# Kernel tuning notes

Hardware: AMD Instinct MI355X
Metric: run time of the kernel (lower is better)

Reference implementation:

```python
import jax, jax.numpy as jnp
import numpy as np


def setup_inputs() -> dict:
    key = jax.random.key(0)
    k1, k2, k3 = jax.random.split(key, 3)
    B, D, F = 4096, 1024, 16384  # batch, input_dim, dict_size
    x = jax.random.normal(k1, (B, D), dtype=jnp.float32)
    W_enc = jax.random.normal(k2, (F, D), dtype=jnp.float32) * (1.0 / np.sqrt(D))
    b_enc = jnp.zeros((F,), dtype=jnp.float32)
    W_dec = jax.random.normal(k3, (D, F), dtype=jnp.float32)
    # decoder columns are unit-normalized (as in _normalize_decoder)
    W_dec = W_dec / jnp.clip(jnp.linalg.norm(W_dec, axis=0, keepdims=True), 1e-8)
    b_dec = jnp.zeros((D,), dtype=jnp.float32)
    return {"x": x, "W_enc": W_enc, "b_enc": b_enc, "W_dec": W_dec, "b_dec": b_dec, "k": 32}


def reference(x, W_enc, b_enc, W_dec, b_dec, k):
    # encode: z_pre = (x - b_dec) @ W_enc^T + b_enc   -> [B, F]
    x_centered = x - b_dec
    z_pre = jnp.einsum('bd,fd->bf', x_centered, W_enc) + b_enc
    # activate: TopK(ReLU(z_pre)) via top_k + relu + scatter
    topk_vals, topk_idx = jax.lax.top_k(z_pre, k)           # [B, k]
    B = z_pre.shape[0]
    rows = jnp.arange(B)[:, None]                            # [B, 1]
    z = jnp.zeros_like(z_pre).at[rows, topk_idx].set(jax.nn.relu(topk_vals))
    # decode: x_hat = z @ W_dec^T + b_dec (dense matmul over sparse z)
    x_hat = jnp.einsum('bf,df->bd', z, W_dec) + b_dec
    return (x_hat, z, z_pre)
```

## Files before the change

### kernel.cpp

```cpp
#include <hip/hip_runtime.h>
#include <cstdint>
#include <cfloat>
#include <cstddef>

#define MAXK 128

typedef __attribute__((ext_vector_type(8))) short bf16x8;
typedef __attribute__((ext_vector_type(4))) float f32x4;

__device__ __forceinline__ void split8(const float4& v0, const float4& v1,
                                       uint4& hp, uint4& lp)
{
    float vv[8] = {v0.x, v0.y, v0.z, v0.w, v1.x, v1.y, v1.z, v1.w};
    unsigned h[8], l[8];
    #pragma unroll
    for (int i = 0; i < 8; ++i) {
        unsigned u  = __float_as_uint(vv[i]);
        unsigned hb = u & 0xFFFF0000u;
        float lf    = vv[i] - __uint_as_float(hb);
        h[i] = u;
        l[i] = __float_as_uint(lf);
    }
    hp.x = (h[0] >> 16) | (h[1] & 0xFFFF0000u);
    hp.y = (h[2] >> 16) | (h[3] & 0xFFFF0000u);
    hp.z = (h[4] >> 16) | (h[5] & 0xFFFF0000u);
    hp.w = (h[6] >> 16) | (h[7] & 0xFFFF0000u);
    lp.x = (l[0] >> 16) | (l[1] & 0xFFFF0000u);
    lp.y = (l[2] >> 16) | (l[3] & 0xFFFF0000u);
    lp.z = (l[4] >> 16) | (l[5] & 0xFFFF0000u);
    lp.w = (l[6] >> 16) | (l[7] & 0xFFFF0000u);
}

__device__ __forceinline__ void gload_lds16(const void* g, void* l)
{
    __builtin_amdgcn_global_load_lds(
        (const __attribute__((address_space(1))) unsigned int*)g,
        (__attribute__((address_space(3))) unsigned int*)l,
        16, 0, 0);
}

__global__ __launch_bounds__(256)
void prep_x_kernel(const float* __restrict__ x, const float* __restrict__ b_dec,
                   ushort* __restrict__ AhiP, ushort* __restrict__ AloP, int D)
{
    const int c   = blockIdx.x * 256 + threadIdx.x;
    const int t   = c >> 9;
    const int wc  = c & 511;
    const int rl  = wc >> 2;
    const int pkc = wc & 3;
    const int kc  = (pkc - (rl >> 1)) & 3;
    const int nkb = D >> 5;
    const int band = t / nkb, kblk = t - band * nkb;
    const int row = band * 128 + rl;
    const int k0  = kblk * 32 + kc * 8;

    const float* src = x + (size_t)row * D + k0;
    float4 v0 = *(const float4*)(src);
    float4 v1 = *(const float4*)(src + 4);
    const float* bd = b_dec + k0;
    float4 d0 = *(const float4*)(bd);
    float4 d1 = *(const float4*)(bd + 4);
    v0.x -= d0.x; v0.y -= d0.y; v0.z -= d0.z; v0.w -= d0.w;
    v1.x -= d1.x; v1.y -= d1.y; v1.z -= d1.z; v1.w -= d1.w;
    uint4 hp, lp;
    split8(v0, v1, hp, lp);
    const size_t off = (size_t)t * 4096 + (size_t)wc * 8;
    *(uint4*)&AhiP[off] = hp;
    *(uint4*)&AloP[off] = lp;
}

__global__ __launch_bounds__(256)
void prep_w_kernel(const float* __restrict__ Wenc,
                   ushort* __restrict__ WhiP, ushort* __restrict__ WloP, int D)
{
    const int c   = blockIdx.x * 256 + threadIdx.x;
    const int t   = c >> 10;
    const int wc  = c & 1023;
    const int rl  = wc >> 2;
    const int pkc = wc & 3;
    const int kc  = (pkc - (rl >> 1)) & 3;
    const int nkb = D >> 5;
    const int fband = t / nkb, kblk = t - fband * nkb;
    const int f   = fband * 256 + rl;
    const int k0  = kblk * 32 + kc * 8;

    const float* src = Wenc + (size_t)f * D + k0;
    float4 v0 = *(const float4*)(src);
    float4 v1 = *(const float4*)(src + 4);
    uint4 hp, lp;
    split8(v0, v1, hp, lp);
    const size_t off = (size_t)t * 8192 + (size_t)wc * 8;
    *(uint4*)&WhiP[off] = hp;
    *(uint4*)&WloP[off] = lp;
}

__global__ __launch_bounds__(256, 2)
void encode_gemm_pre(const ushort* __restrict__ AhiP, const ushort* __restrict__ AloP,
                     const ushort* __restrict__ WhiP, const ushort* __restrict__ WloP,
                     const float* __restrict__ b_enc, float* __restrict__ z_pre,
                     int D, int F)
{
    __shared__ ushort AsHi[4096];
    __shared__ ushort AsLo[4096];
    __shared__ ushort BsHi[8192];
    __shared__ ushort BsLo[8192];

    const int tid = threadIdx.x;
    const int bm  = blockIdx.y * 128;
    const int bn  = blockIdx.x * 256;

    const int lane = tid & 63;
    const int w    = tid >> 6;
    const int wm   = (w >> 1) * 64;
    const int wn   = (w & 1) * 128;
    const int fr   = lane & 15;
    const int q    = lane >> 4;
    const int nkb  = D >> 5;

    int aoff[4], boff[8];
    #pragma unroll
    for (int mi = 0; mi < 4; ++mi) {
        const int r = wm + mi * 16 + fr;
        aoff[mi] = r * 32 + (((q + (r >> 1)) & 3) * 8);
    }
    #pragma unroll
    for (int ni = 0; ni < 8; ++ni) {
        const int r = wn + ni * 16 + fr;
        boff[ni] = r * 32 + (((q + (r >> 1)) & 3) * 8);
    }

    f32x4 acc[4][8];
    #pragma unroll
    for (int mi = 0; mi < 4; ++mi)
        #pragma unroll
        for (int ni = 0; ni < 8; ++ni)
            acc[mi][ni] = (f32x4){0.f, 0.f, 0.f, 0.f};

    const char* aHi = (const char*)AhiP + (size_t)blockIdx.y * nkb * 8192;
    const char* aLo = (const char*)AloP + (size_t)blockIdx.y * nkb * 8192;
    const char* bHi = (const char*)WhiP + (size_t)blockIdx.x * nkb * 16384;
    const char* bLo = (const char*)WloP + (size_t)blockIdx.x * nkb * 16384;
    const int la16 = lane * 16;

    for (int kb = 0; kb < nkb; ++kb) {
        const char* pa = aHi + (size_t)kb * 8192;
        const char* pl = aLo + (size_t)kb * 8192;
        const char* pb = bHi + (size_t)kb * 16384;
        const char* pm = bLo + (size_t)kb * 16384;

        #pragma unroll
        for (int c = 0; c < 2; ++c) {
            const int off = (w * 2 + c) * 1024;
            gload_lds16(pa + off + la16, (char*)AsHi + off);
            gload_lds16(pl + off + la16, (char*)AsLo + off);
        }
        #pragma unroll
        for (int c = 0; c < 4; ++c) {
            const int off = (w * 4 + c) * 1024;
            gload_lds16(pb + off + la16, (char*)BsHi + off);
            gload_lds16(pm + off + la16, (char*)BsLo + off);
        }
        asm volatile("s_waitcnt vmcnt(0)" ::: "memory");
        __syncthreads();

        bf16x8 ahi[4], alo[4];
        #pragma unroll
        for (int mi = 0; mi < 4; ++mi) {
            ahi[mi] = *(const bf16x8*)&AsHi[aoff[mi]];
            alo[mi] = *(const bf16x8*)&AsLo[aoff[mi]];
        }
        #pragma unroll
        for (int ni = 0; ni < 8; ++ni) {
            bf16x8 bhi = *(const bf16x8*)&BsHi[boff[ni]];
            bf16x8 blo = *(const bf16x8*)&BsLo[boff[ni]];
            #pragma unroll
            for (int mi = 0; mi < 4; ++mi) {
                acc[mi][ni] = __builtin_amdgcn_mfma_f32_16x16x32_bf16(alo[mi], bhi, acc[mi][ni], 0, 0, 0);
                acc[mi][ni] = __builtin_amdgcn_mfma_f32_16x16x32_bf16(ahi[mi], blo, acc[mi][ni], 0, 0, 0);
                acc[mi][ni] = __builtin_amdgcn_mfma_f32_16x16x32_bf16(ahi[mi], bhi, acc[mi][ni], 0, 0, 0);
            }
        }
        __syncthreads();
    }

    #pragma unroll
    for (int ni = 0; ni < 8; ++ni) {
        const int col = bn + wn + ni * 16 + fr;
        const float be = b_enc[col];
        #pragma unroll
        for (int mi = 0; mi < 4; ++mi) {
            const int rbase = bm + wm + mi * 16 + q * 4;
            float* dst = z_pre + (size_t)rbase * F + col;
            #pragma unroll
            for (int r = 0; r < 4; ++r)
                dst[(size_t)r * F] = acc[mi][ni][r] + be;
        }
    }
}

__global__ __launch_bounds__(256, 2)
void encode_gemm_bf16x3(const float* __restrict__ x, const float* __restrict__ Wenc,
                        const float* __restrict__ b_enc, const float* __restrict__ b_dec,
                        float* __restrict__ z_pre, int D, int F)
{
    constexpr int BM = 128, BN = 256, BK = 32;
    __shared__ ushort AsHi[BM * BK];
    __shared__ ushort AsLo[BM * BK];
    __shared__ ushort BsHi[BN * BK];
    __shared__ ushort BsLo[BN * BK];

    const int tid = threadIdx.x;
    const int bm  = blockIdx.y * BM;
    const int bn  = blockIdx.x * BN;

    const int lane = tid & 63;
    const int w    = tid >> 6;
    const int wm   = (w >> 1) * 64;
    const int wn   = (w & 1) * 128;
    const int fr   = lane & 15;
    const int q    = lane >> 4;

    int aoff[4], boff[8];
    #pragma unroll
    for (int mi = 0; mi < 4; ++mi) {
        const int r = wm + mi * 16 + fr;
        aoff[mi] = r * 32 + (((q + (r >> 1)) & 3) * 8);
    }
    #pragma unroll
    for (int ni = 0; ni < 8; ++ni) {
        const int r = wn + ni * 16 + fr;
        boff[ni] = r * 32 + (((q + (r >> 1)) & 3) * 8);
    }

    f32x4 acc[4][8];
    #pragma unroll
    for (int mi = 0; mi < 4; ++mi)
        #pragma unroll
        for (int ni = 0; ni < 8; ++ni)
            acc[mi][ni] = (f32x4){0.f, 0.f, 0.f, 0.f};

    for (int k0 = 0; k0 < D; k0 += BK) {
        #pragma unroll
        for (int j = 0; j < 2; ++j) {
            const int task = tid + 256 * j;
            const int row = task >> 2, kc = task & 3;
            const float* src = x + (size_t)(bm + row) * D + k0 + kc * 8;
            float4 v0 = *(const float4*)(src);
            float4 v1 = *(const float4*)(src + 4);
            const float* bd = b_dec + k0 + kc * 8;
            float4 d0 = *(const float4*)(bd);
            float4 d1 = *(const float4*)(bd + 4);
            v0.x -= d0.x; v0.y -= d0.y; v0.z -= d0.z; v0.w -= d0.w;
            v1.x -= d1.x; v1.y -= d1.y; v1.z -= d1.z; v1.w -= d1.w;
            uint4 hp, lp;
            split8(v0, v1, hp, lp);
            const int off = row * 32 + (((kc + (row >> 1)) & 3) * 8);
            *(uint4*)&AsHi[off] = hp;
            *(uint4*)&AsLo[off] = lp;
        }
        #pragma unroll
        for (int j = 0; j < 4; ++j) {
            const int task = tid + 256 * j;
            const int row = task >> 2, kc = task & 3;
            const float* src = Wenc + (size_t)(bn + row) * D + k0 + kc * 8;
            float4 v0 = *(const float4*)(src);
            float4 v1 = *(const float4*)(src + 4);
            uint4 hp, lp;
            split8(v0, v1, hp, lp);
            const int off = row * 32 + (((kc + (row >> 1)) & 3) * 8);
            *(uint4*)&BsHi[off] = hp;
            *(uint4*)&BsLo[off] = lp;
        }
        __syncthreads();

        bf16x8 ahi[4], alo[4];
        #pragma unroll
        for (int mi = 0; mi < 4; ++mi) {
            ahi[mi] = *(const bf16x8*)&AsHi[aoff[mi]];
            alo[mi] = *(const bf16x8*)&AsLo[aoff[mi]];
        }
        #pragma unroll
        for (int ni = 0; ni < 8; ++ni) {
            bf16x8 bhi = *(const bf16x8*)&BsHi[boff[ni]];
            bf16x8 blo = *(const bf16x8*)&BsLo[boff[ni]];
            #pragma unroll
            for (int mi = 0; mi < 4; ++mi) {
                acc[mi][ni] = __builtin_amdgcn_mfma_f32_16x16x32_bf16(alo[mi], bhi, acc[mi][ni], 0, 0, 0);
                acc[mi][ni] = __builtin_amdgcn_mfma_f32_16x16x32_bf16(ahi[mi], blo, acc[mi][ni], 0, 0, 0);
                acc[mi][ni] = __builtin_amdgcn_mfma_f32_16x16x32_bf16(ahi[mi], bhi, acc[mi][ni], 0, 0, 0);
            }
        }
        __syncthreads();
    }

    #pragma unroll
    for (int ni = 0; ni < 8; ++ni) {
        const int col = bn + wn + ni * 16 + fr;
        const float be = b_enc[col];
        #pragma unroll
        for (int mi = 0; mi < 4; ++mi) {
            const int rbase = bm + wm + mi * 16 + q * 4;
            float* dst = z_pre + (size_t)rbase * F + col;
            #pragma unroll
            for (int r = 0; r < 4; ++r)
                dst[(size_t)r * F] = acc[mi][ni][r] + be;
        }
    }
}

__device__ __forceinline__ unsigned fkey(float f)
{
    unsigned u = __float_as_uint(f);
    return u ^ ((unsigned)((int)u >> 31) | 0x80000000u);
}
__device__ __forceinline__ float finv(unsigned k)
{
    unsigned u = (k & 0x80000000u) ? (k ^ 0x80000000u) : ~k;
    return __uint_as_float(u);
}

__device__ __forceinline__ float exact_zpre(const float* __restrict__ xr,
                                            const float* __restrict__ Wenc,
                                            const float* __restrict__ b_enc,
                                            const float* __restrict__ b_dec,
                                            int f, int D, int ln)
{
    const float* wr = Wenc + (size_t)f * D;
    float s = 0.f;
    for (int d = ln * 4; d < D; d += 256) {
        float4 xv = *(const float4*)(xr + d);
        float4 bd = *(const float4*)(b_dec + d);
        float4 wv4 = *(const float4*)(wr + d);
        s = fmaf(xv.x - bd.x, wv4.x, s);
        s = fmaf(xv.y - bd.y, wv4.y, s);
        s = fmaf(xv.z - bd.z, wv4.z, s);
        s = fmaf(xv.w - bd.w, wv4.w, s);
    }
    #pragma unroll
    for (int o = 32; o > 0; o >>= 1) s += __shfl_down(s, o, 64);
    return s + b_enc[f];
}

#define DLT 4e-3f

template <int NVEC>
__global__ __launch_bounds__(256)
void topk_fast(const float* __restrict__ z_pre, float* __restrict__ z,
               float* __restrict__ ws_vals, int* __restrict__ ws_idx,
               const int* __restrict__ k_ptr,
               const float* __restrict__ x, const float* __restrict__ Wenc,
               const float* __restrict__ b_enc, const float* __restrict__ b_dec,
               int F, int D)
{
    const int row = blockIdx.x;
    const int t   = threadIdx.x;
    const int k   = *k_ptr;
    const int nv4 = F >> 2;
    const int wv_id = t >> 6, ln = t & 63;

    __shared__ ushort keys[16384];
    __shared__ float  cand_v[256];
    __shared__ int    cand_i[256];
    __shared__ unsigned char cand_sel[256];
    __shared__ int    bnd[128];
    __shared__ float  s2w[4];
    __shared__ int    hist4[4][256];
    __shared__ int    waveTot[4];
    __shared__ int    s_bin, s_above;
    __shared__ int    n_c_s, n_b_s, c_hi_s, out_cnt, cnt_tau_s, bad_s;
    __shared__ unsigned vk_key;

    if (t == 0) {
        n_c_s = 0; n_b_s = 0; c_hi_s = 0; out_cnt = 0; cnt_tau_s = 0; bad_s = 0;
        vk_key = 0xFFFFFFFFu;
    }

    const float*  zrow = z_pre + (size_t)row * F;
    const float4* src  = (const float4*)zrow;

    float s2 = 0.f;
    #pragma unroll
    for (int i = 0; i < NVEC; ++i) {
        const int p = t + 256 * i;
        if (p < nv4) {
            const float4 v = src[p];
            const unsigned k0 = fkey(v.x) >> 16;
            const unsigned k1 = fkey(v.y) >> 16;
            const unsigned k2 = fkey(v.z) >> 16;
            const unsigned k3 = fkey(v.w) >> 16;
            uint2 pk;
            pk.x = k0 | (k1 << 16);
            pk.y = k2 | (k3 << 16);
            *(uint2*)&keys[p * 4] = pk;
            s2 = fmaf(v.x, v.x, s2);
            s2 = fmaf(v.y, v.y, s2);
            s2 = fmaf(v.z, v.z, s2);
            s2 = fmaf(v.w, v.w, s2);
        }
    }
    #pragma unroll
    for (int o = 32; o > 0; o >>= 1) s2 += __shfl_down(s2, o, 64);
    if (ln == 0) s2w[wv_id] = s2;
    __syncthreads();

    const float sigma = sqrtf((s2w[0] + s2w[1] + s2w[2] + s2w[3]) / (float)F);
    int c0 = 4 * k; if (c0 < 64) c0 = 64; if (c0 > 192) c0 = 192;
    const float qq  = (float)c0 / (float)F;
    const float tt  = sqrtf(-2.f * logf(qq));
    const float phi = tt - (2.30753f + 0.27061f * tt) /
                           (1.f + 0.99229f * tt + 0.04481f * tt * tt);
    const float tau = sigma * phi;
    const unsigned tk = fkey(tau) >> 16;
    const unsigned tkey16 = (tk >= 2) ? (tk - 2) : 0;

    const int nU = nv4 * 2;
    const unsigned* keysU = (const unsigned*)keys;
    for (int j = t; j < nU; j += 256) {
        const unsigned pr = keysU[j];
        const unsigned ka = pr & 0xFFFFu, kb = pr >> 16;
        if (ka > tkey16) { const int s = atomicAdd(&n_c_s, 1); if (s < 256) cand_i[s] = 2 * j; }
        if (kb > tkey16) { const int s = atomicAdd(&n_c_s, 1); if (s < 256) cand_i[s] = 2 * j + 1; }
    }
    __syncthreads();

    if (t == 0 && (n_c_s > 256 || !(tau > 0.1f))) bad_s = 1;
    const int n_c = min(n_c_s, 256);

    float myv = 0.f;
    if (t < n_c) {
        myv = zrow[cand_i[t]];
        cand_v[t] = myv;
        if (myv > tau) atomicAdd(&cnt_tau_s, 1);
    }
    __syncthreads();
    if (t == 0 && cnt_tau_s < k) bad_s = 1;

    cand_sel[t] = 0;
    if (t < n_c) {
        int gt = 0;
        for (int j = 0; j < n_c; ++j) gt += (cand_v[j] > myv);
        if (gt <= k - 1) atomicMin(&vk_key, fkey(myv));
    }
    __syncthreads();

    const float vkv = finv(vk_key);
    if (t < n_c) {
        if (myv > vkv + DLT) {
            cand_sel[t] = 2;
            atomicAdd(&c_hi_s, 1);
        } else if (myv > vkv - DLT) {
            const int sb = atomicAdd(&n_b_s, 1);
            if (sb < 128) bnd[sb] = t;
        }
    }
    __syncthreads();
    if (t == 0 && n_b_s > 128) bad_s = 1;
    __syncthreads();

    if (!bad_s) {
        const int n_b = n_b_s;
        const float* xr = x + (size_t)row * D;
        for (int b2 = wv_id; b2 < n_b; b2 += 4) {
            const int c = bnd[b2];
            const float ex = exact_zpre(xr, Wenc, b_enc, b_dec, cand_i[c], D, ln);
            if (ln == 0) cand_v[c] = ex;
        }
        __syncthreads();

        if (t == 0) {
            int need = k - c_hi_s;
            if (need > n_b) need = n_b;
            for (int it = 0; it < need; ++it) {
                int bi = -1; float bv = 0.f;
                for (int b2 = 0; b2 < n_b; ++b2) {
                    const int c = bnd[b2];
                    if (cand_sel[c]) continue;
                    const float v = cand_v[c];
                    if (bi < 0 || v > bv || (v == bv && cand_i[c] < cand_i[bi])) {
                        bi = c; bv = v;
                    }
                }
                if (bi < 0) break;
                cand_sel[bi] = 1;
            }
        }
        __syncthreads();

        float4* dstz = (float4*)(z + (size_t)row * F);
        const float4 zz = make_float4(0.f, 0.f, 0.f, 0.f);
        #pragma unroll
        for (int i = 0; i < NVEC; ++i) {
            const int p = t + 256 * i;
            if (p < nv4) dstz[p] = zz;
        }
        __syncthreads();

        float* wvp = ws_vals + (size_t)row * MAXK;
        int*   wip = ws_idx  + (size_t)row * MAXK;
        if (t < n_c && cand_sel[t]) {
            const float zv = fmaxf(cand_v[t], 0.f);
            z[(size_t)row * F + cand_i[t]] = zv;
            const int s = atomicAdd(&out_cnt, 1);
            if (s < MAXK) { wvp[s] = zv; wip[s] = cand_i[t]; }
        }
        return;
    }

    if (t == 0) { n_c_s = 0; c_hi_s = 0; out_cnt = 0; }
    __syncthreads();

    unsigned prefix = 0;
    int rem = k;
    for (int pass = 0; pass < 2; ++pass) {
        const int shift = 24 - 8 * pass;
        hist4[0][t] = 0; hist4[1][t] = 0; hist4[2][t] = 0; hist4[3][t] = 0;
        __syncthreads();
        for (int j = t; j < F; j += 256) {
            const unsigned key = fkey(zrow[j]);
            const bool inb = (pass == 0) || ((key >> (shift + 8)) == prefix);
            if (inb) atomicAdd(&hist4[wv_id][(key >> shift) & 255], 1);
        }
        __syncthreads();
        const int cnt = hist4[0][t] + hist4[1][t] + hist4[2][t] + hist4[3][t];
        int s = cnt;
        #pragma unroll
        for (int off = 1; off < 64; off <<= 1) {
            const int tmp = __shfl_down(s, off, 64);
            if (ln + off < 64) s += tmp;
        }
        if (ln == 0) waveTot[wv_id] = s;
        __syncthreads();
        int add = 0;
        #pragma unroll
        for (int w2 = 0; w2 < 4; ++w2)
            if (w2 > wv_id) add += waveTot[w2];
        const int sfx = s + add;
        const int nxt = sfx - cnt;
        if (sfx >= rem && nxt < rem) { s_bin = t; s_above = nxt; }
        __syncthreads();
        rem -= s_above;
        prefix = (prefix << 8) | (unsigned)s_bin;
        __syncthreads();
    }

    const float hiT = finv((prefix << 16) | 0xFFFFu) + DLT;
    const float loT = finv(prefix << 16) - DLT;

    for (int j = t; j < F; j += 256) {
        const float v = zrow[j];
        if (v > hiT) atomicAdd(&c_hi_s, 1);
        else if (v > loT) {
            const int s = atomicAdd(&n_c_s, 1);
            if (s < 256) { cand_i[s] = j; cand_sel[s] = 0; }
        }
    }
    __syncthreads();
    const int n_c2 = min(n_c_s, 256);

    {
        const float* xr = x + (size_t)row * D;
        for (int c = wv_id; c < n_c2; c += 4) {
            const float ex = exact_zpre(xr, Wenc, b_enc, b_dec, cand_i[c], D, ln);
            if (ln == 0) cand_v[c] = ex;
        }
    }
    __syncthreads();

    if (t == 0) {
        int need = k - c_hi_s;
        if (need > n_c2) need = n_c2;
        for (int it = 0; it < need; ++it) {
            int bi = -1; float bv = 0.f;
            for (int c = 0; c < n_c2; ++c) {
                if (cand_sel[c]) continue;
                const float v = cand_v[c];
                if (bi < 0 || v > bv || (v == bv && cand_i[c] < cand_i[bi])) {
                    bi = c; bv = v;
                }
            }
            if (bi < 0) break;
            cand_sel[bi] = 1;
        }
    }
    __syncthreads();

    {
        float4* dstz = (float4*)(z + (size_t)row * F);
        const float4 zz = make_float4(0.f, 0.f, 0.f, 0.f);
        #pragma unroll
        for (int i = 0; i < NVEC; ++i) {
            const int p = t + 256 * i;
            if (p < nv4) dstz[p] = zz;
        }
    }
    __syncthreads();

    float* wvp = ws_vals + (size_t)row * MAXK;
    int*   wip = ws_idx  + (size_t)row * MAXK;
    for (int j = t; j < F; j += 256) {
        const float v = zrow[j];
        if (v > hiT) {
            const float zv = fmaxf(v, 0.f);
            z[(size_t)row * F + j] = zv;
            const int s = atomicAdd(&out_cnt, 1);
            if (s < MAXK) { wvp[s] = zv; wip[s] = j; }
        }
    }
    if (t < n_c2 && cand_sel[t]) {
        const float zv = fmaxf(cand_v[t], 0.f);
        z[(size_t)row * F + cand_i[t]] = zv;
        const int s = atomicAdd(&out_cnt, 1);
        if (s < MAXK) { wvp[s] = zv; wip[s] = cand_i[t]; }
    }
}

template <int NVEC>
__global__ __launch_bounds__(256)
void topk_kernel(const float* __restrict__ z_pre, float* __restrict__ z,
                 float* __restrict__ ws_vals, int* __restrict__ ws_idx,
                 const int* __restrict__ k_ptr,
                 const float* __restrict__ x, const float* __restrict__ Wenc,
                 const float* __restrict__ b_enc, const float* __restrict__ b_dec,
                 int F, int D)
{
    const int row = blockIdx.x;
    const int t   = threadIdx.x;
    const int k   = *k_ptr;
    const int nv4 = F >> 2;
    const int wv_id = t >> 6;
    const int ln    = t & 63;

    const float4* src = (const float4*)(z_pre + (size_t)row * F);
    float4 vals[NVEC];
    #pragma unroll
    for (int i = 0; i < NVEC; ++i) {
        const int p = t + 256 * i;
        if (p < nv4) vals[i] = src[p];
        else         vals[i] = make_float4(-FLT_MAX, -FLT_MAX, -FLT_MAX, -FLT_MAX);
    }

    __shared__ int hist[4][256];
    __shared__ int waveTot[4];
    __shared__ int s_bin, s_above;
    __shared__ int c_hi_s, n_c_s, out_cnt;
    __shared__ int cand_idx[128];
    __shared__ float cand_val[128];
    __shared__ unsigned char cand_sel[128];

    unsigned prefix = 0;
    int rem = k;

    #pragma unroll
    for (int pass = 0; pass < 2; ++pass) {
        const int shift = 24 - 8 * pass;
        hist[0][t] = 0; hist[1][t] = 0; hist[2][t] = 0; hist[3][t] = 0;
        __syncthreads();
        #pragma unroll
        for (int i = 0; i < NVEC; ++i) {
            const float* vv = (const float*)&vals[i];
            #pragma unroll
            for (int j = 0; j < 4; ++j) {
                const unsigned key = fkey(vv[j]);
                const bool inb = (pass == 0) || ((key >> (shift + 8)) == prefix);
                if (inb) atomicAdd(&hist[wv_id][(key >> shift) & 255], 1);
            }
        }
        __syncthreads();
        const int cnt = hist[0][t] + hist[1][t] + hist[2][t] + hist[3][t];
        int s = cnt;
        #pragma unroll
        for (int off = 1; off < 64; off <<= 1) {
            const int tmp = __shfl_down(s, off, 64);
            if (ln + off < 64) s += tmp;
        }
        if (ln == 0) waveTot[wv_id] = s;
        __syncthreads();
        int add = 0;
        #pragma unroll
        for (int w2 = 0; w2 < 4; ++w2)
            if (w2 > wv_id) add += waveTot[w2];
        const int sfx = s + add;
        const int nxt = sfx - cnt;
        if (sfx >= rem && nxt < rem) { s_bin = t; s_above = nxt; }
        __syncthreads();
        rem -= s_above;
        prefix = (prefix << 8) | (unsigned)s_bin;
        __syncthreads();
    }

    const unsigned keyLo = prefix << 16;
    const unsigned keyHi = keyLo | 0xFFFFu;
    const float dlt = 1e-3f;
    const float hiThr = finv(keyHi) + dlt;
    const float loThr = finv(keyLo) - dlt;

    if (t == 0) { c_hi_s = 0; n_c_s = 0; out_cnt = 0; }
    __syncthreads();

    #pragma unroll
    for (int i = 0; i < NVEC; ++i) {
        const float* vv = (const float*)&vals[i];
        #pragma unroll
        for (int j = 0; j < 4; ++j) {
            const float v = vv[j];
            if (v > hiThr) {
                atomicAdd(&c_hi_s, 1);
            } else if (v > loThr) {
                const int s = atomicAdd(&n_c_s, 1);
                if (s < 128) { cand_idx[s] = (t + 256 * i) * 4 + j; cand_sel[s] = 0; }
            }
        }
    }
    __syncthreads();

    const int n_c = min(n_c_s, 128);

    {
        const float* xr = x + (size_t)row * D;
        for (int c = wv_id; c < n_c; c += 4) {
            const float ex = exact_zpre(xr, Wenc, b_enc, b_dec, cand_idx[c], D, ln);
            if (ln == 0) cand_val[c] = ex;
        }
    }
    __syncthreads();

    if (t == 0) {
        int need = k - c_hi_s;
        if (need > n_c) need = n_c;
        for (int it = 0; it < need; ++it) {
            int bi = -1; float bv = 0.f;
            for (int c = 0; c < n_c; ++c) {
                if (cand_sel[c]) continue;
                const float v = cand_val[c];
                if (bi < 0 || v > bv || (v == bv && cand_idx[c] < cand_idx[bi])) {
                    bi = c; bv = v;
                }
            }
            if (bi < 0) break;
            cand_sel[bi] = 1;
        }
    }
    __syncthreads();

    float4* dstz = (float4*)(z + (size_t)row * F);
    float*  wv   = ws_vals + (size_t)row * MAXK;
    int*    wi   = ws_idx  + (size_t)row * MAXK;

    #pragma unroll
    for (int i = 0; i < NVEC; ++i) {
        const int p4 = t + 256 * i;
        if (p4 < nv4) {
            const float* vv = (const float*)&vals[i];
            float4 outv;
            float* ov = (float*)&outv;
            #pragma unroll
            for (int j = 0; j < 4; ++j) {
                const int pos = p4 * 4 + j;
                const float v = vv[j];
                float zv = 0.f;
                bool sel = false;
                if (v > hiThr) {
                    zv = fmaxf(v, 0.f); sel = true;
                } else if (v > loThr) {
                    for (int c = 0; c < n_c; ++c) {
                        if (cand_idx[c] == pos) {
                            if (cand_sel[c]) { zv = fmaxf(cand_val[c], 0.f); sel = true; }
                            break;
                        }
                    }
                }
                ov[j] = zv;
                if (sel) {
                    const int s = atomicAdd(&out_cnt, 1);
                    if (s < MAXK) { wv[s] = zv; wi[s] = pos; }
                }
            }
            dstz[p4] = outv;
        }
    }
}

__global__ __launch_bounds__(256)
void transpose_kernel(const float* __restrict__ in, float* __restrict__ out,
                      int R, int C)
{
    __shared__ float tile[32][33];
    const int c0 = blockIdx.x * 32;
    const int r0 = blockIdx.y * 32;
    const int tx = threadIdx.x & 31;
    const int ty = threadIdx.x >> 5;

    #pragma unroll
    for (int i = ty; i < 32; i += 8) {
        const int r = r0 + i, c = c0 + tx;
        tile[i][tx] = (r < R && c < C) ? in[(size_t)r * C + c] : 0.f;
    }
    __syncthreads();
    #pragma unroll
    for (int i = ty; i < 32; i += 8) {
        const int c = c0 + i, r = r0 + tx;
        if (c < C && r < R) out[(size_t)c * R + r] = tile[tx][i];
    }
}

__global__ __launch_bounds__(256)
void decode_kernel(const float* __restrict__ WdT, const float* __restrict__ wvals,
                   const int* __restrict__ widx, const float* __restrict__ b_dec,
                   float* __restrict__ x_hat, const int* __restrict__ k_ptr, int D)
{
    __shared__ float sv[MAXK];
    __shared__ int   si[MAXK];
    const int row = blockIdx.x;
    const int t   = threadIdx.x;
    int k = *k_ptr;
    if (k > MAXK) k = MAXK;

    if (t < MAXK) {
        sv[t] = wvals[(size_t)row * MAXK + t];
        si[t] = widx [(size_t)row * MAXK + t];
    }
    __syncthreads();

    for (int d0 = t * 4; d0 < D; d0 += 1024) {
        float4 acc0 = *(const float4*)(b_dec + d0);
        float4 acc1 = make_float4(0.f, 0.f, 0.f, 0.f);
        int j = 0;
        for (; j + 2 <= k; j += 2) {
            const float v0 = sv[j],     v1 = sv[j + 1];
            const int   f0 = si[j],     f1 = si[j + 1];
            const float4 w0 = *(const float4*)(WdT + (size_t)f0 * D + d0);
            const float4 w1 = *(const float4*)(WdT + (size_t)f1 * D + d0);
            acc0.x = fmaf(v0, w0.x, acc0.x);
            acc0.y = fmaf(v0, w0.y, acc0.y);
            acc0.z = fmaf(v0, w0.z, acc0.z);
            acc0.w = fmaf(v0, w0.w, acc0.w);
            acc1.x = fmaf(v1, w1.x, acc1.x);
            acc1.y = fmaf(v1, w1.y, acc1.y);
            acc1.z = fmaf(v1, w1.z, acc1.z);
            acc1.w = fmaf(v1, w1.w, acc1.w);
        }
        if (j < k) {
            const float v0 = sv[j];
            const float4 w0 = *(const float4*)(WdT + (size_t)si[j] * D + d0);
            acc0.x = fmaf(v0, w0.x, acc0.x);
            acc0.y = fmaf(v0, w0.y, acc0.y);
            acc0.z = fmaf(v0, w0.z, acc0.z);
            acc0.w = fmaf(v0, w0.w, acc0.w);
        }
        acc0.x += acc1.x; acc0.y += acc1.y; acc0.z += acc1.z; acc0.w += acc1.w;
        *(float4*)(x_hat + (size_t)row * D + d0) = acc0;
    }
}

extern "C" void kernel_launch(void* const* d_in, const int* in_sizes, int n_in,
                              void* d_out, int out_size, void* d_ws, size_t ws_size,
                              hipStream_t stream)
{
    const float* x     = (const float*)d_in[0];
    const float* W_enc = (const float*)d_in[1];
    const float* b_enc = (const float*)d_in[2];
    const float* W_dec = (const float*)d_in[3];
    const float* b_dec = (const float*)d_in[4];
    const int*   k_ptr = (const int*)d_in[5];

    const int F = in_sizes[2];
    const int D = in_sizes[4];
    const int B = in_sizes[0] / D;

    float* x_hat = (float*)d_out;
    float* z     = x_hat + (size_t)B * D;
    float* z_pre = z + (size_t)B * F;

    float* WdT = (float*)d_ws;
    float* wv  = WdT + (size_t)F * D;
    int*   wi  = (int*)(wv + (size_t)B * MAXK);
    char*  extra = (char*)(wi + (size_t)B * MAXK);

    const size_t base_need  = (size_t)F * D * 4 + (size_t)B * MAXK * 8;
    const size_t extra_need = (size_t)B * D * 4 + (size_t)F * D * 4;
    const bool use_pre = (ws_size >= base_need + extra_need) &&
                         (D % 32 == 0) && (B % 128 == 0) && (F % 256 == 0);

    if (use_pre) {
        ushort* AhiP = (ushort*)extra;
        ushort* AloP = AhiP + (size_t)B * D;
        ushort* WhiP = AloP + (size_t)B * D;
        ushort* WloP = WhiP + (size_t)F * D;

        prep_x_kernel<<<(B * (D / 8)) / 256, 256, 0, stream>>>(x, b_dec, AhiP, AloP, D);
        prep_w_kernel<<<(F * (D / 8)) / 256, 256, 0, stream>>>(W_enc, WhiP, WloP, D);
        encode_gemm_pre<<<dim3(F / 256, B / 128), 256, 0, stream>>>(
            AhiP, AloP, WhiP, WloP, b_enc, z_pre, D, F);
    } else {
        encode_gemm_bf16x3<<<dim3(F / 256, B / 128), 256, 0, stream>>>(
            x, W_enc, b_enc, b_dec, z_pre, D, F);
    }

    transpose_kernel<<<dim3((F + 31) / 32, (D + 31) / 32), 256, 0, stream>>>(
        W_dec, WdT, D, F);

    const int nv4  = F / 4;
    const int nvec = (nv4 + 255) / 256;
    const bool fastok = (F <= 16384) && ((F & 3) == 0);

    if (fastok) {
        if (nvec <= 4)
            topk_fast<4><<<B, 256, 0, stream>>>(z_pre, z, wv, wi, k_ptr, x, W_enc, b_enc, b_dec, F, D);
        else if (nvec <= 8)
            topk_fast<8><<<B, 256, 0, stream>>>(z_pre, z, wv, wi, k_ptr, x, W_enc, b_enc, b_dec, F, D);
        else
            topk_fast<16><<<B, 256, 0, stream>>>(z_pre, z, wv, wi, k_ptr, x, W_enc, b_enc, b_dec, F, D);
    } else {
        if (nvec <= 8)
            topk_kernel<8><<<B, 256, 0, stream>>>(z_pre, z, wv, wi, k_ptr, x, W_enc, b_enc, b_dec, F, D);
        else if (nvec <= 16)
            topk_kernel<16><<<B, 256, 0, stream>>>(z_pre, z, wv, wi, k_ptr, x, W_enc, b_enc, b_dec, F, D);
        else
            topk_kernel<32><<<B, 256, 0, stream>>>(z_pre, z, wv, wi, k_ptr, x, W_enc, b_enc, b_dec, F, D);
    }

    decode_kernel<<<B, 256, 0, stream>>>(WdT, wv, wi, b_dec, x_hat, k_ptr, D);
}
```

Measured before the change: 1.119 ms.

## Add double-buffered encode GEMM with XCD-aware block swizzle; fuse z zeroing into load

```diff
diff --git a/kernel.cpp b/kernel.cpp
--- a/kernel.cpp
+++ b/kernel.cpp
@@ -92,6 +92,130 @@
     const size_t off = (size_t)t * 8192 + (size_t)wc * 8;
     *(uint4*)&WhiP[off] = hp;
     *(uint4*)&WloP[off] = lp;
+}
+
+__global__ __launch_bounds__(256, 1)
+void encode_gemm_db(const ushort* __restrict__ AhiP, const ushort* __restrict__ AloP,
+                    const ushort* __restrict__ WhiP, const ushort* __restrict__ WloP,
+                    const float* __restrict__ b_enc, float* __restrict__ z_pre,
+                    int D, int F, int nbm)
+{
+    __shared__ ushort AsHi0[4096], AsLo0[4096];
+    __shared__ ushort BsHi0[8192], BsLo0[8192];
+    __shared__ ushort AsHi1[4096], AsLo1[4096];
+    __shared__ ushort BsHi1[8192], BsLo1[8192];
+
+    const int tid = threadIdx.x;
+    const int nwg = gridDim.x;
+    int lb = blockIdx.x;
+    if ((nwg & 7) == 0) {
+        const int per = nwg >> 3;
+        lb = (blockIdx.x & 7) * per + (blockIdx.x >> 3);
+    }
+    const int bm = (lb % nbm) * 128;
+    const int bn = (lb / nbm) * 256;
+
+    const int lane = tid & 63;
+    const int w    = tid >> 6;
+    const int wm   = (w >> 1) * 64;
+    const int wn   = (w & 1) * 128;
+    const int fr   = lane & 15;
+    const int q    = lane >> 4;
+    const int nkb  = D >> 5;
+
+    int aoff[4], boff[8];
+    #pragma unroll
+    for (int mi = 0; mi < 4; ++mi) {
+        const int r = wm + mi * 16 + fr;
+        aoff[mi] = r * 32 + (((q + (r >> 1)) & 3) * 8);
+    }
+    #pragma unroll
+    for (int ni = 0; ni < 8; ++ni) {
+        const int r = wn + ni * 16 + fr;
+        boff[ni] = r * 32 + (((q + (r >> 1)) & 3) * 8);
+    }
+
+    f32x4 acc[4][8];
+    #pragma unroll
+    for (int mi = 0; mi < 4; ++mi)
+        #pragma unroll
+        for (int ni = 0; ni < 8; ++ni)
+            acc[mi][ni] = (f32x4){0.f, 0.f, 0.f, 0.f};
+
+    const char* aHi = (const char*)AhiP + (size_t)(bm >> 7) * nkb * 8192;
+    const char* aLo = (const char*)AloP + (size_t)(bm >> 7) * nkb * 8192;
+    const char* bHi = (const char*)WhiP + (size_t)(bn >> 8) * nkb * 16384;
+    const char* bLo = (const char*)WloP + (size_t)(bn >> 8) * nkb * 16384;
+    const int la16 = lane * 16;
+
+    auto stage = [&](int kb, ushort* dAH, ushort* dAL, ushort* dBH, ushort* dBL) {
+        const char* pa = aHi + (size_t)kb * 8192;
+        const char* pl = aLo + (size_t)kb * 8192;
+        const char* pb = bHi + (size_t)kb * 16384;
+        const char* pm = bLo + (size_t)kb * 16384;
+        #pragma unroll
+        for (int c = 0; c < 2; ++c) {
+            const int off = (w * 2 + c) * 1024;
+            gload_lds16(pa + off + la16, (char*)dAH + off);
+            gload_lds16(pl + off + la16, (char*)dAL + off);
+        }
+        #pragma unroll
+        for (int c = 0; c < 4; ++c) {
+            const int off = (w * 4 + c) * 1024;
+            gload_lds16(pb + off + la16, (char*)dBH + off);
+            gload_lds16(pm + off + la16, (char*)dBL + off);
+        }
+    };
+
+    auto compute = [&](const ushort* sAH, const ushort* sAL,
+                       const ushort* sBH, const ushort* sBL) {
+        bf16x8 ahi[4], alo[4];
+        #pragma unroll
+        for (int mi = 0; mi < 4; ++mi) {
+            ahi[mi] = *(const bf16x8*)&sAH[aoff[mi]];
+            alo[mi] = *(const bf16x8*)&sAL[aoff[mi]];
+        }
+        #pragma unroll
+        for (int ni = 0; ni < 8; ++ni) {
+            bf16x8 bhi = *(const bf16x8*)&sBH[boff[ni]];
+            bf16x8 blo = *(const bf16x8*)&sBL[boff[ni]];
+            #pragma unroll
+            for (int mi = 0; mi < 4; ++mi) {
+                acc[mi][ni] = __builtin_amdgcn_mfma_f32_16x16x32_bf16(alo[mi], bhi, acc[mi][ni], 0, 0, 0);
+                acc[mi][ni] = __builtin_amdgcn_mfma_f32_16x16x32_bf16(ahi[mi], blo, acc[mi][ni], 0, 0, 0);
+                acc[mi][ni] = __builtin_amdgcn_mfma_f32_16x16x32_bf16(ahi[mi], bhi, acc[mi][ni], 0, 0, 0);
+            }
+        }
+    };
+
+    stage(0, AsHi0, AsLo0, BsHi0, BsLo0);
+    asm volatile("s_waitcnt vmcnt(0)" ::: "memory");
+    __syncthreads();
+
+    for (int kb = 0; kb < nkb; kb += 2) {
+        if (kb + 1 < nkb) stage(kb + 1, AsHi1, AsLo1, BsHi1, BsLo1);
+        compute(AsHi0, AsLo0, BsHi0, BsLo0);
+        asm volatile("s_waitcnt vmcnt(0)" ::: "memory");
+        __syncthreads();
+        if (kb + 2 < nkb) stage(kb + 2, AsHi0, AsLo0, BsHi0, BsLo0);
+        compute(AsHi1, AsLo1, BsHi1, BsLo1);
+        asm volatile("s_waitcnt vmcnt(0)" ::: "memory");
+        __syncthreads();
+    }
+
+    #pragma unroll
+    for (int ni = 0; ni < 8; ++ni) {
+        const int col = bn + wn + ni * 16 + fr;
+        const float be = b_enc[col];
+        #pragma unroll
+        for (int mi = 0; mi < 4; ++mi) {
+            const int rbase = bm + wm + mi * 16 + q * 4;
+            float* dst = z_pre + (size_t)rbase * F + col;
+            #pragma unroll
+            for (int r = 0; r < 4; ++r)
+                dst[(size_t)r * F] = acc[mi][ni][r] + be;
+        }
+    }
 }
 
 __global__ __launch_bounds__(256, 2)
@@ -377,6 +501,8 @@
 
     const float*  zrow = z_pre + (size_t)row * F;
     const float4* src  = (const float4*)zrow;
+    float4* dstz = (float4*)(z + (size_t)row * F);
+    const float4 zz = make_float4(0.f, 0.f, 0.f, 0.f);
 
     float s2 = 0.f;
     #pragma unroll
@@ -384,6 +510,7 @@
         const int p = t + 256 * i;
         if (p < nv4) {
             const float4 v = src[p];
+            dstz[p] = zz;
             const unsigned k0 = fkey(v.x) >> 16;
             const unsigned k1 = fkey(v.y) >> 16;
             const unsigned k2 = fkey(v.z) >> 16;
@@ -486,15 +613,6 @@
         }
         __syncthreads();
 
-        float4* dstz = (float4*)(z + (size_t)row * F);
-        const float4 zz = make_float4(0.f, 0.f, 0.f, 0.f);
-        #pragma unroll
-        for (int i = 0; i < NVEC; ++i) {
-            const int p = t + 256 * i;
-            if (p < nv4) dstz[p] = zz;
-        }
-        __syncthreads();
-
         float* wvp = ws_vals + (size_t)row * MAXK;
         int*   wip = ws_idx  + (size_t)row * MAXK;
         if (t < n_c && cand_sel[t]) {
@@ -585,12 +703,11 @@
     __syncthreads();
 
     {
-        float4* dstz = (float4*)(z + (size_t)row * F);
-        const float4 zz = make_float4(0.f, 0.f, 0.f, 0.f);
+        const float4 z4 = make_float4(0.f, 0.f, 0.f, 0.f);
         #pragma unroll
         for (int i = 0; i < NVEC; ++i) {
             const int p = t + 256 * i;
-            if (p < nv4) dstz[p] = zz;
+            if (p < nv4) dstz[p] = z4;
         }
     }
     __syncthreads();
@@ -889,8 +1006,15 @@
 
         prep_x_kernel<<<(B * (D / 8)) / 256, 256, 0, stream>>>(x, b_dec, AhiP, AloP, D);
         prep_w_kernel<<<(F * (D / 8)) / 256, 256, 0, stream>>>(W_enc, WhiP, WloP, D);
-        encode_gemm_pre<<<dim3(F / 256, B / 128), 256, 0, stream>>>(
-            AhiP, AloP, WhiP, WloP, b_enc, z_pre, D, F);
+
+        const int nbm = B / 128, nbn = F / 256;
+        if (D % 64 == 0) {
+            encode_gemm_db<<<nbm * nbn, 256, 0, stream>>>(
+                AhiP, AloP, WhiP, WloP, b_enc, z_pre, D, F, nbm);
+        } else {
+            encode_gemm_pre<<<dim3(nbn, nbm), 256, 0, stream>>>(
+                AhiP, AloP, WhiP, WloP, b_enc, z_pre, D, F);
+        }
     } else {
         encode_gemm_bf16x3<<<dim3(F / 256, B / 128), 256, 0, stream>>>(
             x, W_enc, b_enc, b_dec, z_pre, D, F);
```

Result: slower. 1.312 ms (+17.3%).
